# Kernel optimization log

Measured on AMD Instinct MI355X. Metric: run time of the kernel, lower is better.

Reference implementation:

```python
import jax, jax.numpy as jnp
import numpy as np
import math

B, S, D, H = 8, 1024, 512, 8
AD = D // H  # attn_dim = 64


def setup_inputs() -> dict:
    key = jax.random.key(0)
    ks = jax.random.split(key, 16)
    def lin(i):
        w = jax.random.normal(ks[i], (D, D), jnp.float32) * (1.0 / math.sqrt(D))
        b = jnp.zeros((D,), jnp.float32)
        return w, b
    Wq, bq = lin(0); Wk, bk = lin(1); Wv, bv = lin(2); Wr, br = lin(3); Wo, bo = lin(4)
    return {
        "query": jax.random.normal(ks[5], (B, S, D), jnp.float32),
        "key": jax.random.normal(ks[6], (B, S, D), jnp.float32),
        "value": jax.random.normal(ks[7], (B, S, D), jnp.float32),
        "relpos": jax.random.normal(ks[8], (B, S, D), jnp.float32),
        "key_padding_mask": jnp.zeros((B, S), dtype=bool),
        "Wq": Wq, "bq": bq, "Wk": Wk, "bk": bk, "Wv": Wv, "bv": bv,
        "Wr": Wr, "br": br, "Wo": Wo, "bo": bo,
        "U_bias": jax.random.normal(ks[9], (H, AD), jnp.float32) * 0.05,
        "V_bias": jax.random.normal(ks[10], (H, AD), jnp.float32) * 0.05,
    }


def _rel_shift(x):
    # x: (b, h, q, k). Transformer-XL shift trick.
    b, h, q, k = x.shape
    xp = jnp.pad(x, ((0, 0), (0, 0), (0, 0), (1, 0)))  # (b,h,q,k+1)
    xp = xp.reshape(b, h, k + 1, q)
    return xp[:, :, 1:].reshape(b, h, q, k)


def reference(query, key, value, relpos, key_padding_mask,
              Wq, bq, Wk, bk, Wv, bv, Wr, br, Wo, bo, U_bias, V_bias):
    b = query.shape[0]
    Q = (query @ Wq.T + bq).reshape(b, -1, H, AD)    # (b,q,h,d)
    K = (key @ Wk.T + bk).reshape(b, -1, H, AD)      # (b,k,h,d)
    V = (value @ Wv.T + bv).reshape(b, -1, H, AD)    # (b,k,h,d)
    R = (relpos @ Wr.T + br).reshape(b, -1, H, AD)   # (b,k,h,d)

    AC = jnp.einsum('bqhd,bkhd->bhqk', Q + U_bias, K)
    BD = _rel_shift(jnp.einsum('bqhd,bkhd->bhqk', Q + V_bias, R))
    scores = (AC + BD) / math.sqrt(AD)               # (b,h,q,k)

    bias = jnp.where(key_padding_mask, jnp.float32(-1e9), jnp.float32(0.0))
    scores = scores + bias[:, None, None, :]
    attn = jax.nn.softmax(scores, axis=-1)           # (b,h,q,k)

    Hc = jnp.einsum('bhqk,bkhd->bqhd', attn, V).reshape(b, -1, D)
    out = Hc @ Wo.T + bo
    attn_weights = attn.reshape(b * H, attn.shape[2], attn.shape[3])
    return out, attn_weights
```

## Files before the change

kernel.cpp:

```cpp
#include <hip/hip_runtime.h>


typedef __attribute__((ext_vector_type(8))) short bf16x8;
typedef __attribute__((ext_vector_type(8))) float f32x8;
typedef __attribute__((ext_vector_type(4))) float f32x4;

#define MFMA16(a, b, c) __builtin_amdgcn_mfma_f32_16x16x32_bf16((a), (b), (c), 0, 0, 0)

__device__ __forceinline__ float b2f(short s) {
    union { unsigned u; float f; } v;
    v.u = ((unsigned)(unsigned short)s) << 16;
    return v.f;
}
__device__ __forceinline__ short f2b(float f) {
    union { float f; unsigned u; } v;
    v.f = f;
    unsigned r = v.u + 0x7fffu + ((v.u >> 16) & 1u);
    return (short)(r >> 16);
}
__device__ __forceinline__ bf16x8 ld8(const void* p, long idx, int isbf) {
    if (isbf) return *(const bf16x8*)((const short*)p + idx);
    f32x8 f = *(const f32x8*)((const float*)p + idx);
    bf16x8 r;
#pragma unroll
    for (int j = 0; j < 8; j++) r[j] = f2b(f[j]);
    return r;
}
__device__ __forceinline__ float ld1(const void* p, long idx, int isbf) {
    return isbf ? b2f(((const short*)p)[idx]) : ((const float*)p)[idx];
}

__global__ void sniff_dtype(const unsigned* __restrict__ q, int* __restrict__ flag) {
    if (threadIdx.x == 0 && blockIdx.x == 0) {
        int hits = 0;
        for (int i = 0; i < 64; i++) {
            unsigned e = (q[i] >> 7) & 0xFFu;
            hits += (e >= 100u && e <= 140u) ? 1 : 0;
        }
        *flag = (hits > 40) ? 1 : 0;
    }
}

struct CvtArgs { const void* src[8]; };
__global__ __launch_bounds__(256) void convert_all(
        CvtArgs a, short* __restrict__ dst, const int* __restrict__ flag) {
    const int isbf = *flag;
    const long NP = 4194304, WN = 262144;
    const int bid = blockIdx.x;
    int seg;
    long dstoff, eoff;
    if (bid < 8192) {
        seg = bid >> 11;
        dstoff = (long)seg * NP;
        eoff = (long)(bid & 2047) * 2048 + threadIdx.x * 8;
    } else {
        seg = 4 + ((bid - 8192) >> 7);
        dstoff = 4 * NP + (long)(seg - 4) * WN;
        eoff = (long)((bid - 8192) & 127) * 2048 + threadIdx.x * 8;
    }
    const void* s = a.src[seg];
    if (isbf) {
        *(bf16x8*)(dst + dstoff + eoff) = *(const bf16x8*)((const short*)s + eoff);
    } else {
        f32x8 f = *(const f32x8*)((const float*)s + eoff);
        bf16x8 r;
#pragma unroll
        for (int j = 0; j < 8; j++) r[j] = f2b(f[j]);
        *(bf16x8*)(dst + dstoff + eoff) = r;
    }
}

__device__ __forceinline__ void gemm_body(
        const void* __restrict__ A, const void* __restrict__ W,
        const void* __restrict__ bias, void* __restrict__ C,
        int bm, int bn, int isbf, int a_isbf, int w_isbf, int c_f32) {
    const int w = threadIdx.x >> 6, lane = threadIdx.x & 63;
    const int m0 = bm * 128 + (w >> 1) * 64;
    const int n0 = bn * 128 + (w & 1) * 64;
    const int lr = lane & 15, lk8 = (lane >> 4) * 8;

    f32x4 acc[4][4] = {};
    for (int kk = 0; kk < 512; kk += 32) {
        bf16x8 a[4], bfr[4];
#pragma unroll
        for (int r = 0; r < 4; r++)
            a[r] = ld8(A, (long)(m0 + r * 16 + lr) * 512 + kk + lk8, a_isbf);
#pragma unroll
        for (int c = 0; c < 4; c++)
            bfr[c] = ld8(W, (long)(n0 + c * 16 + lr) * 512 + kk + lk8, w_isbf);
#pragma unroll
        for (int r = 0; r < 4; r++)
#pragma unroll
            for (int c = 0; c < 4; c++)
                acc[r][c] = MFMA16(a[r], bfr[c], acc[r][c]);
    }
    const int orow = (lane >> 4) * 4;
#pragma unroll
    for (int c = 0; c < 4; c++) {
        const int col = n0 + c * 16 + lr;
        const float bv = ld1(bias, col, isbf);
#pragma unroll
        for (int r = 0; r < 4; r++)
#pragma unroll
            for (int j = 0; j < 4; j++) {
                const long off = (long)(m0 + r * 16 + orow + j) * 512 + col;
                const float v = acc[r][c][j] + bv;
                if (c_f32) ((float*)C)[off] = v;
                else       ((short*)C)[off] = f2b(v);
            }
    }
}

struct P4 { const void* bias[4]; short* C[4]; };
__global__ __launch_bounds__(256) void proj4(
        const short* __restrict__ Sc, P4 p4, const int* __restrict__ flag) {
    const int isbf = *flag;
    const long NP = 4194304, WN = 262144;
    const int p = blockIdx.x;
    const int xcd = p & 7, u = p >> 3;
    const int op = xcd >> 1;
    const int idx = (xcd & 1) * 128 + u;
    gemm_body(Sc + (long)op * NP, Sc + 4 * NP + (long)op * WN,
              p4.bias[op], p4.C[op], idx & 63, idx >> 6, isbf, 1, 1, 0);
}

__global__ __launch_bounds__(256) void gemm_xwT64(
        const short* __restrict__ A, const void* __restrict__ W,
        const void* __restrict__ bias, float* __restrict__ C,
        const int* __restrict__ flag, int w_dyn) {
    const int isbf = *flag;
    const int w_isbf = w_dyn ? isbf : 1;
    const int bm = blockIdx.x & 127;
    const int bn = blockIdx.x >> 7;
    const int w = threadIdx.x >> 6, lane = threadIdx.x & 63;
    const int m0 = bm * 64 + w * 16;
    const int n0 = bn * 64;
    const int lr = lane & 15, lk8 = (lane >> 4) * 8;

    f32x4 acc[4] = {};
    for (int kk = 0; kk < 512; kk += 32) {
        bf16x8 a = *(const bf16x8*)(A + (long)(m0 + lr) * 512 + kk + lk8);
        bf16x8 bfr[4];
#pragma unroll
        for (int c = 0; c < 4; c++)
            bfr[c] = ld8(W, (long)(n0 + c * 16 + lr) * 512 + kk + lk8, w_isbf);
#pragma unroll
        for (int c = 0; c < 4; c++)
            acc[c] = MFMA16(a, bfr[c], acc[c]);
    }
    const int orow = (lane >> 4) * 4;
#pragma unroll
    for (int c = 0; c < 4; c++) {
        const int col = n0 + c * 16 + lr;
        const float bv = ld1(bias, col, isbf);
#pragma unroll
        for (int j = 0; j < 4; j++)
            C[(long)(m0 + orow + j) * 512 + col] = acc[c][j] + bv;
    }
}

__global__ __launch_bounds__(256) void transpose_v(
        const short* __restrict__ Vp, short* __restrict__ Vt) {
    __shared__ short T[64][72];
    const int bh = blockIdx.x >> 2;
    const int kq = blockIdx.x & 3;
    const int b = bh >> 3, h = bh & 7;
    const int t = threadIdx.x;
    const short* src = Vp + (long)b * 1024 * 512 + h * 64;
    short* dst = Vt + (long)bh * 65536;
    for (int kb = kq * 4; kb < kq * 4 + 4; kb++) {
        __syncthreads();
#pragma unroll
        for (int it = 0; it < 2; it++) {
            const int row = it * 32 + (t >> 3);
            const int col = (t & 7) * 8;
            *(bf16x8*)&T[row][col] =
                *(const bf16x8*)(src + (long)(kb * 64 + row) * 512 + col);
        }
        __syncthreads();
#pragma unroll
        for (int it = 0; it < 2; it++) {
            const int d = it * 32 + (t >> 3);
            const int kk = (t & 7) * 8;
            bf16x8 v;
#pragma unroll
            for (int e = 0; e < 8; e++) v[e] = T[kk + e][d];
            *(bf16x8*)(dst + (long)d * 1024 + kb * 64 + kk) = v;
        }
    }
}

__global__ __launch_bounds__(512, 4) void attn_fused(
        const short* __restrict__ Q, const short* __restrict__ K,
        const short* __restrict__ R, const short* __restrict__ Vt,
        const void* __restrict__ Ub, const void* __restrict__ Vb,
        const unsigned char* __restrict__ mask,
        float* __restrict__ attn_out, short* __restrict__ Hc,
        const int* __restrict__ flag) {
    __shared__ __align__(16) short Esh[2][17 * 1032];
    __shared__ float redmx[2][4][16];
    __shared__ float redsm[2][4][16];
    const int isbf = *flag;

    const int p = blockIdx.x;
    const int xcd = p & 7, u = p >> 3;
    const int bh = (u >> 5) * 8 + xcd;
    const int qt = u & 31;
    const int b = bh >> 3, h = bh & 7;
    const int q0 = qt * 32;
    const int w = threadIdx.x >> 6, lane = threadIdx.x & 63;
    const int g = w >> 2, wq = w & 3;
    const int qg0 = q0 + g * 16;
    const int lr = lane & 15, lg = lane >> 4, lk8 = lg * 8;

    const long kvbase = (long)(b * 1024) * 512 + h * 64;
    short* E = &Esh[g][0];

    {
        bf16x8 aV0[2], aV1[2];
#pragma unroll
        for (int ks = 0; ks < 2; ks++) {
            const int dof = ks * 32 + lk8;
            bf16x8 qv = *(const bf16x8*)(Q + (long)(b * 1024 + qg0 + lr) * 512 + h * 64 + dof);
            int qr = qg0 + 16 + lr;
            if (qr > 1023) qr = 1023;
            bf16x8 qv1 = *(const bf16x8*)(Q + (long)(b * 1024 + qr) * 512 + h * 64 + dof);
#pragma unroll
            for (int j = 0; j < 8; j++) {
                const float vbj = ld1(Vb, h * 64 + dof + j, isbf);
                aV0[ks][j] = f2b(b2f(qv[j]) + vbj);
                aV1[ks][j] = f2b(b2f(qv1[j]) + vbj);
            }
        }
#pragma unroll 4
        for (int tt = 0; tt < 16; tt++) {
            const int k0 = (wq * 16 + tt) * 16;
            f32x4 e0 = {}, e1 = {};
#pragma unroll
            for (int ks = 0; ks < 2; ks++) {
                bf16x8 rf = *(const bf16x8*)(R + kvbase + (long)(k0 + lr) * 512 + ks * 32 + lk8);
                e0 = MFMA16(aV0[ks], rf, e0);
                e1 = MFMA16(aV1[ks], rf, e1);
            }
            const int jcol = k0 + lr;
#pragma unroll
            for (int j = 0; j < 4; j++)
                E[(lg * 4 + j) * 1032 + jcol] = f2b(e0[j]);
            if (lg == 0) E[16 * 1032 + jcol] = f2b(e1[0]);
        }
    }
    __syncthreads();

    f32x4 acc[16];
    {
        bf16x8 aU[2];
#pragma unroll
        for (int ks = 0; ks < 2; ks++) {
            const int dof = ks * 32 + lk8;
            bf16x8 qv = *(const bf16x8*)(Q + (long)(b * 1024 + qg0 + lr) * 512 + h * 64 + dof);
#pragma unroll
            for (int j = 0; j < 8; j++)
                aU[ks][j] = f2b(b2f(qv[j]) + ld1(Ub, h * 64 + dof + j, isbf));
        }
        const unsigned char* mrow = mask + b * 1024;
#pragma unroll
        for (int tt = 0; tt < 16; tt++) {
            const int k0 = (wq * 16 + tt) * 16;
            f32x4 a = {};
#pragma unroll
            for (int ks = 0; ks < 2; ks++) {
                bf16x8 kf = *(const bf16x8*)(K + kvbase + (long)(k0 + lr) * 512 + ks * 32 + lk8);
                a = MFMA16(aU[ks], kf, a);
            }
            const int c = k0 + lr;
            const float mbias = mrow[c] ? -1e9f : 0.0f;
#pragma unroll
            for (int j = 0; j < 4; j++) {
                const int r = lg * 4 + j;
                const int dq = c - qg0 - r;
                const int idx = r * 1032 + dq + ((dq <= 0) ? 1023 : 1030);
                float bd = b2f(E[idx]);
                if (dq == 1) bd = 0.0f;
                a[j] = (a[j] + bd) * 0.125f + mbias;
            }
            acc[tt] = a;
        }
    }

    float mx[4], sm[4];
#pragma unroll
    for (int j = 0; j < 4; j++) {
        float m = -1e30f;
#pragma unroll
        for (int tt = 0; tt < 16; tt++) m = fmaxf(m, acc[tt][j]);
#pragma unroll
        for (int off = 1; off <= 8; off <<= 1) m = fmaxf(m, __shfl_xor(m, off));
        mx[j] = m;
    }
    if (lr == 0) {
#pragma unroll
        for (int j = 0; j < 4; j++) redmx[g][wq][lg * 4 + j] = mx[j];
    }
    __syncthreads();
#pragma unroll
    for (int j = 0; j < 4; j++) {
        float m = redmx[g][0][lg * 4 + j];
#pragma unroll
        for (int ww = 1; ww < 4; ww++) m = fmaxf(m, redmx[g][ww][lg * 4 + j]);
        mx[j] = m;
        sm[j] = 0.0f;
    }
#pragma unroll
    for (int tt = 0; tt < 16; tt++)
#pragma unroll
        for (int j = 0; j < 4; j++) {
            const float e = __expf(acc[tt][j] - mx[j]);
            acc[tt][j] = e;
            sm[j] += e;
        }
#pragma unroll
    for (int j = 0; j < 4; j++) {
#pragma unroll
        for (int off = 1; off <= 8; off <<= 1) sm[j] += __shfl_xor(sm[j], off);
    }
    if (lr == 0) {
#pragma unroll
        for (int j = 0; j < 4; j++) redsm[g][wq][lg * 4 + j] = sm[j];
    }
    __syncthreads();
    float inv[4];
#pragma unroll
    for (int j = 0; j < 4; j++) {
        float s = redsm[g][0][lg * 4 + j];
#pragma unroll
        for (int ww = 1; ww < 4; ww++) s += redsm[g][ww][lg * 4 + j];
        inv[j] = 1.0f / s;
    }

    short* P = E;
#pragma unroll
    for (int tt = 0; tt < 16; tt++) {
        const int c = (wq * 16 + tt) * 16 + lr;
#pragma unroll
        for (int j = 0; j < 4; j++)
            P[(lg * 4 + j) * 1048 + c] = f2b(acc[tt][j] * inv[j]);
    }
    __syncthreads();

    float* abase = attn_out + ((long)bh * 1024 + qg0) * 1024;
#pragma unroll
    for (int rr = 0; rr < 4; rr++) {
        const int r = wq * 4 + rr;
#pragma unroll
        for (int half = 0; half < 2; half++) {
            const bf16x8 pv8 = *(const bf16x8*)&P[r * 1048 + half * 512 + lane * 8];
            f32x4 lo, hi;
#pragma unroll
            for (int e = 0; e < 4; e++) { lo[e] = b2f(pv8[e]); hi[e] = b2f(pv8[4 + e]); }
            float* dst = abase + (long)r * 1024 + half * 512 + lane * 8;
            *(f32x4*)dst = lo;
            *(f32x4*)(dst + 4) = hi;
        }
    }

    f32x4 oacc = {};
    const short* vtb = Vt + (long)bh * 65536 + (long)(wq * 16 + lr) * 1024;
    for (int ks = 0; ks < 32; ks++) {
        const bf16x8 aa = *(const bf16x8*)&P[lr * 1048 + ks * 32 + lk8];
        const bf16x8 bb = *(const bf16x8*)(vtb + ks * 32 + lk8);
        oacc = MFMA16(aa, bb, oacc);
    }
#pragma unroll
    for (int j = 0; j < 4; j++)
        Hc[(long)(b * 1024 + qg0 + lg * 4 + j) * 512 + h * 64 + wq * 16 + lr] = f2b(oacc[j]);
}

extern "C" void kernel_launch(void* const* d_in, const int* in_sizes, int n_in,
                              void* d_out, int out_size, void* d_ws, size_t ws_size,
                              hipStream_t stream) {
    const void* query  = d_in[0];
    const void* key    = d_in[1];
    const void* value  = d_in[2];
    const void* relpos = d_in[3];
    const unsigned char* mask = (const unsigned char*)d_in[4];
    const void* Wq = d_in[5];  const void* bq = d_in[6];
    const void* Wk = d_in[7];  const void* bk = d_in[8];
    const void* Wv = d_in[9];  const void* bv = d_in[10];
    const void* Wr = d_in[11]; const void* br = d_in[12];
    const void* Wo = d_in[13]; const void* bo = d_in[14];
    const void* Ub = d_in[15]; const void* Vb = d_in[16];

    float* out  = (float*)d_out;
    float* attn = out + (long)4194304;

    const long NP = 4194304;
    short* ws = (short*)d_ws;
    short* Kp = ws;
    short* Vp = ws + NP;
    short* Rp = ws + 2 * NP;
    int* flag = (int*)(ws + 3 * NP);
    short* Qp = (short*)out;
    short* Vt = (short*)out + NP;
    short* Hc = Vp;
    short* Sc = (short*)attn;

    sniff_dtype<<<1, 64, 0, stream>>>((const unsigned*)query, flag);

    CvtArgs ca;
    ca.src[0] = query; ca.src[1] = key; ca.src[2] = value; ca.src[3] = relpos;
    ca.src[4] = Wq; ca.src[5] = Wk; ca.src[6] = Wv; ca.src[7] = Wr;
    convert_all<<<8704, 256, 0, stream>>>(ca, Sc, flag);

    P4 p4;
    p4.bias[0] = bq; p4.C[0] = Qp;
    p4.bias[1] = bk; p4.C[1] = Kp;
    p4.bias[2] = bv; p4.C[2] = Vp;
    p4.bias[3] = br; p4.C[3] = Rp;
    proj4<<<1024, 256, 0, stream>>>(Sc, p4, flag);

    transpose_v<<<256, 256, 0, stream>>>(Vp, Vt);

    attn_fused<<<2048, 512, 0, stream>>>(Qp, Kp, Rp, Vt, Ub, Vb, mask,
                                         attn, Hc, flag);

    gemm_xwT64<<<1024, 256, 0, stream>>>(Hc, Wo, bo, out, flag, 1);
}
```

Baseline: 386.2 us.

## Fuse input fp32-to-bf16 conversion into QKVR projection GEMM with LDS-staged A tiles

Measured after the change: 384.0 us. About the same (-0.6%).

```diff
diff --git a/kernel.cpp b/kernel.cpp
--- a/kernel.cpp
+++ b/kernel.cpp
@@ -41,95 +41,71 @@
     }
 }
 
-struct CvtArgs { const void* src[8]; };
-__global__ __launch_bounds__(256) void convert_all(
+struct CvtArgs { const void* src[4]; };
+__global__ __launch_bounds__(256) void convert_w(
         CvtArgs a, short* __restrict__ dst, const int* __restrict__ flag) {
     const int isbf = *flag;
-    const long NP = 4194304, WN = 262144;
-    const int bid = blockIdx.x;
-    int seg;
-    long dstoff, eoff;
-    if (bid < 8192) {
-        seg = bid >> 11;
-        dstoff = (long)seg * NP;
-        eoff = (long)(bid & 2047) * 2048 + threadIdx.x * 8;
-    } else {
-        seg = 4 + ((bid - 8192) >> 7);
-        dstoff = 4 * NP + (long)(seg - 4) * WN;
-        eoff = (long)((bid - 8192) & 127) * 2048 + threadIdx.x * 8;
-    }
+    const long WN = 262144;
+    const int seg = blockIdx.x >> 7;
+    const long eoff = (long)(blockIdx.x & 127) * 2048 + threadIdx.x * 8;
     const void* s = a.src[seg];
-    if (isbf) {
-        *(bf16x8*)(dst + dstoff + eoff) = *(const bf16x8*)((const short*)s + eoff);
-    } else {
-        f32x8 f = *(const f32x8*)((const float*)s + eoff);
-        bf16x8 r;
-#pragma unroll
-        for (int j = 0; j < 8; j++) r[j] = f2b(f[j]);
-        *(bf16x8*)(dst + dstoff + eoff) = r;
-    }
-}
-
-__device__ __forceinline__ void gemm_body(
-        const void* __restrict__ A, const void* __restrict__ W,
-        const void* __restrict__ bias, void* __restrict__ C,
-        int bm, int bn, int isbf, int a_isbf, int w_isbf, int c_f32) {
+    bf16x8 v = ld8(s, eoff, isbf);
+    *(bf16x8*)(dst + seg * WN + eoff) = v;
+}
+
+struct PF { const void* A[4]; const void* bias[4]; short* C[4]; };
+__global__ __launch_bounds__(512, 2) void proj_fused(
+        PF pf, const short* __restrict__ Wc, const int* __restrict__ flag) {
+    __shared__ short At[128][40];
+    const int isbf = *flag;
+    const long WN = 262144;
+    const int p = blockIdx.x;
+    const int xcd = p & 7;
+    const int op = xcd >> 1;
+    const int bm = (xcd & 1) * 32 + (p >> 3);
+    const void* A = pf.A[op];
+    const short* W = Wc + (long)op * WN;
+
     const int w = threadIdx.x >> 6, lane = threadIdx.x & 63;
-    const int m0 = bm * 128 + (w >> 1) * 64;
-    const int n0 = bn * 128 + (w & 1) * 64;
-    const int lr = lane & 15, lk8 = (lane >> 4) * 8;
-
-    f32x4 acc[4][4] = {};
+    const int rg = w >> 1, ch = w & 1;
+    const int lr = lane & 15, lg = lane >> 4, lk8 = lg * 8;
+    const int srow = threadIdx.x >> 2, scol = (threadIdx.x & 3) * 8;
+
+    f32x4 acc[2][16] = {};
     for (int kk = 0; kk < 512; kk += 32) {
-        bf16x8 a[4], bfr[4];
-#pragma unroll
-        for (int r = 0; r < 4; r++)
-            a[r] = ld8(A, (long)(m0 + r * 16 + lr) * 512 + kk + lk8, a_isbf);
-#pragma unroll
-        for (int c = 0; c < 4; c++)
-            bfr[c] = ld8(W, (long)(n0 + c * 16 + lr) * 512 + kk + lk8, w_isbf);
-#pragma unroll
-        for (int r = 0; r < 4; r++)
-#pragma unroll
-            for (int c = 0; c < 4; c++)
-                acc[r][c] = MFMA16(a[r], bfr[c], acc[r][c]);
-    }
-    const int orow = (lane >> 4) * 4;
-#pragma unroll
-    for (int c = 0; c < 4; c++) {
-        const int col = n0 + c * 16 + lr;
-        const float bv = ld1(bias, col, isbf);
-#pragma unroll
-        for (int r = 0; r < 4; r++)
-#pragma unroll
-            for (int j = 0; j < 4; j++) {
-                const long off = (long)(m0 + r * 16 + orow + j) * 512 + col;
-                const float v = acc[r][c][j] + bv;
-                if (c_f32) ((float*)C)[off] = v;
-                else       ((short*)C)[off] = f2b(v);
-            }
-    }
-}
-
-struct P4 { const void* bias[4]; short* C[4]; };
-__global__ __launch_bounds__(256) void proj4(
-        const short* __restrict__ Sc, P4 p4, const int* __restrict__ flag) {
-    const int isbf = *flag;
-    const long NP = 4194304, WN = 262144;
-    const int p = blockIdx.x;
-    const int xcd = p & 7, u = p >> 3;
-    const int op = xcd >> 1;
-    const int idx = (xcd & 1) * 128 + u;
-    gemm_body(Sc + (long)op * NP, Sc + 4 * NP + (long)op * WN,
-              p4.bias[op], p4.C[op], idx & 63, idx >> 6, isbf, 1, 1, 0);
+        bf16x8 sv = ld8(A, (long)(bm * 128 + srow) * 512 + kk + scol, isbf);
+        *(bf16x8*)&At[srow][scol] = sv;
+        __syncthreads();
+        const bf16x8 a0 = *(const bf16x8*)&At[rg * 32 + lr][lk8];
+        const bf16x8 a1 = *(const bf16x8*)&At[rg * 32 + 16 + lr][lk8];
+#pragma unroll
+        for (int c = 0; c < 16; c++) {
+            const bf16x8 wf = *(const bf16x8*)(W + (long)(ch * 256 + c * 16 + lr) * 512 + kk + lk8);
+            acc[0][c] = MFMA16(a0, wf, acc[0][c]);
+            acc[1][c] = MFMA16(a1, wf, acc[1][c]);
+        }
+        __syncthreads();
+    }
+    const int orow = lg * 4;
+    short* C = pf.C[op];
+#pragma unroll
+    for (int c = 0; c < 16; c++) {
+        const int col = ch * 256 + c * 16 + lr;
+        const float bv = ld1(pf.bias[op], col, isbf);
+#pragma unroll
+        for (int rt = 0; rt < 2; rt++)
+#pragma unroll
+            for (int j = 0; j < 4; j++)
+                C[(long)(bm * 128 + rg * 32 + rt * 16 + orow + j) * 512 + col] =
+                    f2b(acc[rt][c][j] + bv);
+    }
 }
 
 __global__ __launch_bounds__(256) void gemm_xwT64(
         const short* __restrict__ A, const void* __restrict__ W,
         const void* __restrict__ bias, float* __restrict__ C,
-        const int* __restrict__ flag, int w_dyn) {
+        const int* __restrict__ flag) {
     const int isbf = *flag;
-    const int w_isbf = w_dyn ? isbf : 1;
     const int bm = blockIdx.x & 127;
     const int bn = blockIdx.x >> 7;
     const int w = threadIdx.x >> 6, lane = threadIdx.x & 63;
@@ -143,7 +119,7 @@
         bf16x8 bfr[4];
 #pragma unroll
         for (int c = 0; c < 4; c++)
-            bfr[c] = ld8(W, (long)(n0 + c * 16 + lr) * 512 + kk + lk8, w_isbf);
+            bfr[c] = ld8(W, (long)(n0 + c * 16 + lr) * 512 + kk + lk8, isbf);
 #pragma unroll
         for (int c = 0; c < 4; c++)
             acc[c] = MFMA16(a, bfr[c], acc[c]);
@@ -407,21 +383,20 @@
     sniff_dtype<<<1, 64, 0, stream>>>((const unsigned*)query, flag);
 
     CvtArgs ca;
-    ca.src[0] = query; ca.src[1] = key; ca.src[2] = value; ca.src[3] = relpos;
-    ca.src[4] = Wq; ca.src[5] = Wk; ca.src[6] = Wv; ca.src[7] = Wr;
-    convert_all<<<8704, 256, 0, stream>>>(ca, Sc, flag);
-
-    P4 p4;
-    p4.bias[0] = bq; p4.C[0] = Qp;
-    p4.bias[1] = bk; p4.C[1] = Kp;
-    p4.bias[2] = bv; p4.C[2] = Vp;
-    p4.bias[3] = br; p4.C[3] = Rp;
-    proj4<<<1024, 256, 0, stream>>>(Sc, p4, flag);
+    ca.src[0] = Wq; ca.src[1] = Wk; ca.src[2] = Wv; ca.src[3] = Wr;
+    convert_w<<<512, 256, 0, stream>>>(ca, Sc, flag);
+
+    PF pf;
+    pf.A[0] = query;  pf.bias[0] = bq; pf.C[0] = Qp;
+    pf.A[1] = key;    pf.bias[1] = bk; pf.C[1] = Kp;
+    pf.A[2] = value;  pf.bias[2] = bv; pf.C[2] = Vp;
+    pf.A[3] = relpos; pf.bias[3] = br; pf.C[3] = Rp;
+    proj_fused<<<256, 512, 0, stream>>>(pf, Sc, flag);
 
     transpose_v<<<256, 256, 0, stream>>>(Vp, Vt);
 
     attn_fused<<<2048, 512, 0, stream>>>(Qp, Kp, Rp, Vt, Ub, Vb, mask,
                                          attn, Hc, flag);
 
-    gemm_xwT64<<<1024, 256, 0, stream>>>(Hc, Wo, bo, out, flag, 1);
-}
+    gemm_xwT64<<<1024, 256, 0, stream>>>(Hc, Wo, bo, out, flag);
+}
```
